# Kernel optimization log

Hardware: AMD Instinct MI355X
Metric: run time of the kernel (lower is better)

The kernel has to match this reference:

```python
import jax, jax.numpy as jnp
import numpy as np

N, D, C = 4096, 512, 64
MARGIN = 1.0
INF = jnp.float32(1e30)


def setup_inputs() -> dict:
    key = jax.random.key(0)
    k1, k2 = jax.random.split(key)
    embeddings = jax.random.normal(k1, (N, D), dtype=jnp.float32)
    targets = jax.random.randint(k2, (N,), 0, C)
    return {"embeddings": embeddings, "targets": targets}


def _triplet_loss(embeddings, targets, margin=MARGIN):
    # Squared pairwise distances [N, N] (differentiable, used for the loss)
    sq_norms = jnp.sum(embeddings * embeddings, axis=1)
    sq_dist = jnp.maximum(
        sq_norms[:, None] + sq_norms[None, :] - 2.0 * (embeddings @ embeddings.T), 0.0
    )
    # Euclidean distances for mining only (index selection is non-differentiable in torch)
    dist = jnp.sqrt(jax.lax.stop_gradient(sq_dist))

    same = targets[:, None] == targets[None, :]  # [N, N] same-label mask

    # Hardest negative per anchor: argmax_k (d_ap - d_ak + margin) == argmin_k d_ak over negatives
    neg_dist = jnp.where(same, INF, dist)
    n_idx = jnp.argmin(neg_dist, axis=1)   # [N] hardest negative index per anchor
    min_neg = jnp.min(neg_dist, axis=1)    # [N] its euclidean distance

    idx = jnp.arange(dist.shape[0])
    # anchor-positive pairs: same label, a < p (torch.combinations on sorted indices)
    pair_mask = same & (idx[:, None] < idx[None, :])
    # triplet kept only if mined loss (euclidean) strictly positive
    valid = pair_mask & (dist - min_neg[:, None] + margin > 0)

    ap_sq = sq_dist                         # [N, N] squared anchor-positive distances
    an_sq = sq_dist[idx, n_idx]             # [N]   squared anchor-hard-negative distances
    losses = jax.nn.relu(ap_sq - an_sq[:, None] + margin)

    cnt = jnp.sum(valid)
    denom = jnp.maximum(cnt, 1).astype(losses.dtype)
    loss = jnp.sum(jnp.where(valid, losses, 0.0)) / denom

    correct = jnp.sum(valid & (ap_sq < an_sq[:, None]))
    accuracy = correct.astype(jnp.float32) / jnp.maximum(cnt, 1).astype(jnp.float32)
    return loss, accuracy


def reference(embeddings, targets):
    return _triplet_loss(embeddings, targets)
```

## Files before the change

### kernel.cpp

```cpp
#include <hip/hip_runtime.h>

#define N 4096
#define D 512
#define C 64
#define MARGIN 1.0f
#define TILE 128
#define ROWB 128
#define NTILES (N / TILE)
#define NTRI (NTILES * (NTILES + 1) / 2)
#define FINF 3.0e38f
#define SLOTW 16
#define PCAP 1024
#define LOSSB 128

typedef __attribute__((ext_vector_type(8))) short short8;
typedef __attribute__((ext_vector_type(4))) float floatx4;

__device__ __forceinline__ unsigned short f2bf(float f) {
  unsigned int u = __float_as_uint(f);
  u += 0x7FFFu + ((u >> 16) & 1u);
  return (unsigned short)(u >> 16);
}

__device__ __forceinline__ void gload_lds16(const void* g, void* l) {
  __builtin_amdgcn_global_load_lds(
      (const __attribute__((address_space(1))) unsigned int*)g,
      (__attribute__((address_space(3))) unsigned int*)l, 16, 0, 0);
}

__global__ __launch_bounds__(256) void prep_kernel(const float* __restrict__ E,
                                                   unsigned short* __restrict__ Ebf,
                                                   float* __restrict__ norms,
                                                   unsigned int* __restrict__ an_sq_bits,
                                                   unsigned int* __restrict__ accs_u,
                                                   unsigned int* __restrict__ ctrl) {
  const int row = blockIdx.x;
  const int tid = threadIdx.x;
  if (row == N) {
    for (int k = tid; k < C * SLOTW; k += 256) accs_u[k] = 0u;
    if (tid < 2) ctrl[tid] = 0u;
    return;
  }
  if (row < 16) an_sq_bits[row * 256 + tid] = 0x7F800000u;
  const float2 v = reinterpret_cast<const float2*>(E + (size_t)row * D)[tid];
  float s = v.x * v.x + v.y * v.y;
  unsigned int packed = ((unsigned int)f2bf(v.y) << 16) | (unsigned int)f2bf(v.x);
  reinterpret_cast<unsigned int*>(Ebf + (size_t)row * D)[tid] = packed;
  for (int off = 32; off > 0; off >>= 1) s += __shfl_down(s, off);
  __shared__ float wsum[4];
  if ((tid & 63) == 0) wsum[tid >> 6] = s;
  __syncthreads();
  if (tid == 0) norms[row] = wsum[0] + wsum[1] + wsum[2] + wsum[3];
}

__global__ __launch_bounds__(256, 3) void gemm_min_kernel(const unsigned short* __restrict__ Ebf,
                                                          const float* __restrict__ norms,
                                                          const int* __restrict__ targets,
                                                          unsigned int* __restrict__ an_sq_bits,
                                                          uint2* __restrict__ pairs,
                                                          unsigned int* __restrict__ ctrl) {
  const int u = blockIdx.x;
  int i = (int)((sqrtf(8.0f * (float)u + 1.0f) - 1.0f) * 0.5f);
  while ((i + 1) * (i + 2) / 2 <= u) ++i;
  while (i * (i + 1) / 2 > u) --i;
  const int tm = u - i * (i + 1) / 2;
  const int tn = i;

  __shared__ alignas(16) unsigned char As[TILE * ROWB];
  __shared__ alignas(16) unsigned char Bs[TILE * ROWB];
  __shared__ float s_rmin[2][TILE];
  __shared__ float s_cmin[2][TILE];
  __shared__ unsigned int s_pkey[PCAP];
  __shared__ float s_psq[PCAP];
  __shared__ unsigned int s_pcnt, s_pbase;

  const int tid = threadIdx.x;
  const int wave = tid >> 6, lane = tid & 63;
  const int quad = lane >> 4, l16 = lane & 15;
  const int wr = wave >> 1, wc = wave & 1;
  const int rowBase = tm * TILE, colBase = tn * TILE;
  if (tid == 0) s_pcnt = 0u;

  const int lr = lane >> 3;
  const int lq = (lane & 7) ^ lr;
  const int lofs = lr * (D * 2) + lq * 16;
  const unsigned char* gA = (const unsigned char*)Ebf + (size_t)rowBase * (D * 2);
  const unsigned char* gB = (const unsigned char*)Ebf + (size_t)colBase * (D * 2);

  const int swz = l16 & 7;
  int rA[4], rB[4], cq[2];
#pragma unroll
  for (int s = 0; s < 4; s++) {
    rA[s] = (wr * 64 + s * 16 + l16) * ROWB;
    rB[s] = (wc * 64 + s * 16 + l16) * ROWB;
  }
#pragma unroll
  for (int ks = 0; ks < 2; ks++) cq[ks] = ((ks * 4 + quad) ^ swz) * 16;

  floatx4 acc[4][4];
#pragma unroll
  for (int a = 0; a < 4; a++)
#pragma unroll
    for (int b = 0; b < 4; b++) acc[a][b] = (floatx4){0.f, 0.f, 0.f, 0.f};

  for (int k0b = 0; k0b < D * 2; k0b += 128) {
#pragma unroll
    for (int t = 0; t < 4; t++) {
      const int g = wave * 4 + t;
      gload_lds16(gA + (size_t)g * 8 * (D * 2) + lofs + k0b, As + g * 1024);
      gload_lds16(gB + (size_t)g * 8 * (D * 2) + lofs + k0b, Bs + g * 1024);
    }
    __syncthreads();
#pragma unroll
    for (int ks = 0; ks < 2; ks++) {
      short8 af[4], bf[4];
#pragma unroll
      for (int s = 0; s < 4; s++) {
        af[s] = *reinterpret_cast<const short8*>(As + rA[s] + cq[ks]);
        bf[s] = *reinterpret_cast<const short8*>(Bs + rB[s] + cq[ks]);
      }
#pragma unroll
      for (int sm = 0; sm < 4; sm++)
#pragma unroll
        for (int sn = 0; sn < 4; sn++)
          acc[sm][sn] = __builtin_amdgcn_mfma_f32_16x16x32_bf16(af[sm], bf[sn], acc[sm][sn], 0, 0, 0);
    }
    __syncthreads();
  }

  int tcol[4], gcolv[4];
  float ncol[4];
#pragma unroll
  for (int sn = 0; sn < 4; sn++) {
    const int gc = colBase + wc * 64 + sn * 16 + l16;
    gcolv[sn] = gc;
    tcol[sn] = targets[gc];
    ncol[sn] = norms[gc];
  }
  float colmin[4] = {FINF, FINF, FINF, FINF};
#pragma unroll
  for (int sm = 0; sm < 4; sm++) {
#pragma unroll
    for (int r = 0; r < 4; r++) {
      const int rloc = wr * 64 + sm * 16 + quad * 4 + r;
      const int grow = rowBase + rloc;
      const int trow = targets[grow];
      const float nrow = norms[grow];
      float rowmin = FINF;
#pragma unroll
      for (int sn = 0; sn < 4; sn++) {
        const float sq = fmaxf(nrow + ncol[sn] - 2.0f * acc[sm][sn][r], 0.0f);
        if (tcol[sn] != trow) {
          rowmin = fminf(rowmin, sq);
          colmin[sn] = fminf(colmin[sn], sq);
        } else if (grow < gcolv[sn]) {
          const unsigned int idx = atomicAdd(&s_pcnt, 1u);
          if (idx < PCAP) {
            s_pkey[idx] = ((unsigned int)grow << 12) | (unsigned int)gcolv[sn];
            s_psq[idx] = sq;
          } else {
            const unsigned int g = atomicAdd(&ctrl[0], 1u);
            pairs[g] = make_uint2(((unsigned int)grow << 12) | (unsigned int)gcolv[sn],
                                  __float_as_uint(sq));
          }
        }
      }
#pragma unroll
      for (int off = 1; off < 16; off <<= 1) rowmin = fminf(rowmin, __shfl_xor(rowmin, off));
      if (l16 == 0) s_rmin[wc][rloc] = rowmin;
    }
  }
#pragma unroll
  for (int sn = 0; sn < 4; sn++) {
    float cm = colmin[sn];
    cm = fminf(cm, __shfl_xor(cm, 16));
    cm = fminf(cm, __shfl_xor(cm, 32));
    if (quad == 0) s_cmin[wr][wc * 64 + sn * 16 + l16] = cm;
  }
  __syncthreads();
  if (tid < TILE) {
    const float m = fminf(s_rmin[0][tid], s_rmin[1][tid]);
    if (m < FINF) atomicMin(&an_sq_bits[rowBase + tid], __float_as_uint(m));
  } else {
    const int c = tid - TILE;
    const float m = fminf(s_cmin[0][c], s_cmin[1][c]);
    if (m < FINF) atomicMin(&an_sq_bits[colBase + c], __float_as_uint(m));
  }
  const unsigned int npair = min(s_pcnt, (unsigned int)PCAP);
  if (tid == 0) s_pbase = atomicAdd(&ctrl[0], npair);
  __syncthreads();
  for (unsigned int r = tid; r < npair; r += 256)
    pairs[s_pbase + r] = make_uint2(s_pkey[r], __float_as_uint(s_psq[r]));
}

__global__ __launch_bounds__(256) void loss_kernel(const uint2* __restrict__ pairs,
                                                   const unsigned int* __restrict__ an_sq_bits,
                                                   float* __restrict__ accs,
                                                   unsigned int* __restrict__ ctrl,
                                                   float* __restrict__ out) {
  const int tid = threadIdx.x, wave = tid >> 6, lane = tid & 63;
  const unsigned int M = ctrl[0];
  __shared__ float s_sum[4];
  __shared__ unsigned int s_cnt[4], s_cor[4];
  __shared__ int s_last;
  float bsum = 0.f;
  unsigned int bcnt = 0, bcor = 0;
  for (unsigned int r = blockIdx.x * 256 + tid; r < M; r += LOSSB * 256) {
    const uint2 rec = pairs[r];
    const int a = (int)(rec.x >> 12);
    const float sq = __uint_as_float(rec.y);
    const float an = __uint_as_float(an_sq_bits[a]);
    if (sqrtf(sq) - sqrtf(an) + MARGIN > 0.0f) {
      bcnt++;
      bsum += fmaxf(sq - an + MARGIN, 0.0f);
      if (sq < an) bcor++;
    }
  }
#pragma unroll
  for (int off = 32; off > 0; off >>= 1) {
    bsum += __shfl_down(bsum, off);
    bcnt += __shfl_down(bcnt, off);
    bcor += __shfl_down(bcor, off);
  }
  if (lane == 0) { s_sum[wave] = bsum; s_cnt[wave] = bcnt; s_cor[wave] = bcor; }
  __syncthreads();
  if (tid == 0) {
    float* slot = accs + (size_t)(blockIdx.x & (C - 1)) * SLOTW;
    atomicAdd(&slot[0], s_sum[0] + s_sum[1] + s_sum[2] + s_sum[3]);
    atomicAdd((unsigned int*)&slot[1], s_cnt[0] + s_cnt[1] + s_cnt[2] + s_cnt[3]);
    atomicAdd((unsigned int*)&slot[2], s_cor[0] + s_cor[1] + s_cor[2] + s_cor[3]);
    __threadfence();
    s_last = (atomicAdd(&ctrl[1], 1u) == (unsigned int)LOSSB - 1u);
  }
  __syncthreads();
  if (s_last) {
    __threadfence();
    if (tid < C) {
      float sum = __uint_as_float(atomicAdd((unsigned int*)&accs[(size_t)tid * SLOTW + 0], 0u));
      unsigned int cnt = atomicAdd((unsigned int*)&accs[(size_t)tid * SLOTW + 1], 0u);
      unsigned int cor = atomicAdd((unsigned int*)&accs[(size_t)tid * SLOTW + 2], 0u);
#pragma unroll
      for (int off = 32; off > 0; off >>= 1) {
        sum += __shfl_down(sum, off);
        cnt += __shfl_down(cnt, off);
        cor += __shfl_down(cor, off);
      }
      if (tid == 0) {
        const float denom = (float)(cnt > 0u ? cnt : 1u);
        out[0] = sum / denom;
        out[1] = (float)cor / denom;
      }
    }
  }
}

extern "C" void kernel_launch(void* const* d_in, const int* in_sizes, int n_in,
                              void* d_out, int out_size, void* d_ws, size_t ws_size,
                              hipStream_t stream) {
  const float* E = (const float*)d_in[0];
  const int* targets = (const int*)d_in[1];
  float* out = (float*)d_out;
  char* ws = (char*)d_ws;
  size_t off = 0;
  unsigned short* Ebf = (unsigned short*)(ws + off); off += (size_t)N * D * 2;
  float* norms = (float*)(ws + off); off += (size_t)N * 4;
  unsigned int* an_sq = (unsigned int*)(ws + off); off += (size_t)N * 4;
  float* accs = (float*)(ws + off); off += (size_t)C * SLOTW * 4;
  unsigned int* ctrl = (unsigned int*)(ws + off); off += 256;
  uint2* pairs = (uint2*)(ws + off);

  prep_kernel<<<dim3(N + 1), dim3(256), 0, stream>>>(E, Ebf, norms, an_sq, (unsigned int*)accs, ctrl);
  gemm_min_kernel<<<dim3(NTRI), dim3(256), 0, stream>>>(Ebf, norms, targets, an_sq, pairs, ctrl);
  loss_kernel<<<dim3(LOSSB), dim3(256), 0, stream>>>(pairs, an_sq, accs, ctrl, out);
}
```

Before: 95.93 us.

## Fuse bf16 conversion and norm computation into the distance GEMM kernel

Result: slower. 137.8 us (+43.6%).

```diff
diff --git a/kernel.cpp b/kernel.cpp
--- a/kernel.cpp
+++ b/kernel.cpp
@@ -5,13 +5,12 @@
 #define C 64
 #define MARGIN 1.0f
 #define TILE 128
-#define ROWB 128
 #define NTILES (N / TILE)
 #define NTRI (NTILES * (NTILES + 1) / 2)
 #define FINF 3.0e38f
 #define SLOTW 16
 #define PCAP 1024
-#define LOSSB 128
+#define LOSSB 132
 
 typedef __attribute__((ext_vector_type(8))) short short8;
 typedef __attribute__((ext_vector_type(4))) float floatx4;
@@ -21,78 +20,56 @@
   u += 0x7FFFu + ((u >> 16) & 1u);
   return (unsigned short)(u >> 16);
 }
-
-__device__ __forceinline__ void gload_lds16(const void* g, void* l) {
-  __builtin_amdgcn_global_load_lds(
-      (const __attribute__((address_space(1))) unsigned int*)g,
-      (__attribute__((address_space(3))) unsigned int*)l, 16, 0, 0);
-}
-
-__global__ __launch_bounds__(256) void prep_kernel(const float* __restrict__ E,
-                                                   unsigned short* __restrict__ Ebf,
-                                                   float* __restrict__ norms,
-                                                   unsigned int* __restrict__ an_sq_bits,
-                                                   unsigned int* __restrict__ accs_u,
-                                                   unsigned int* __restrict__ ctrl) {
-  const int row = blockIdx.x;
-  const int tid = threadIdx.x;
-  if (row == N) {
-    for (int k = tid; k < C * SLOTW; k += 256) accs_u[k] = 0u;
-    if (tid < 2) ctrl[tid] = 0u;
-    return;
-  }
-  if (row < 16) an_sq_bits[row * 256 + tid] = 0x7F800000u;
-  const float2 v = reinterpret_cast<const float2*>(E + (size_t)row * D)[tid];
-  float s = v.x * v.x + v.y * v.y;
-  unsigned int packed = ((unsigned int)f2bf(v.y) << 16) | (unsigned int)f2bf(v.x);
-  reinterpret_cast<unsigned int*>(Ebf + (size_t)row * D)[tid] = packed;
-  for (int off = 32; off > 0; off >>= 1) s += __shfl_down(s, off);
-  __shared__ float wsum[4];
-  if ((tid & 63) == 0) wsum[tid >> 6] = s;
-  __syncthreads();
-  if (tid == 0) norms[row] = wsum[0] + wsum[1] + wsum[2] + wsum[3];
-}
-
-__global__ __launch_bounds__(256, 3) void gemm_min_kernel(const unsigned short* __restrict__ Ebf,
-                                                          const float* __restrict__ norms,
-                                                          const int* __restrict__ targets,
-                                                          unsigned int* __restrict__ an_sq_bits,
-                                                          uint2* __restrict__ pairs,
-                                                          unsigned int* __restrict__ ctrl) {
+__device__ __forceinline__ unsigned int cvt_pk(float x, float y) {
+  return ((unsigned int)f2bf(y) << 16) | (unsigned int)f2bf(x);
+}
+
+__global__ __launch_bounds__(256, 3) void gemm_fused(const float* __restrict__ E,
+                                                     const int* __restrict__ targets,
+                                                     unsigned int* __restrict__ an_key,
+                                                     uint2* __restrict__ pairs,
+                                                     unsigned int* __restrict__ pcnt,
+                                                     unsigned int* __restrict__ accs_u,
+                                                     unsigned int* __restrict__ ctrl) {
   const int u = blockIdx.x;
-  int i = (int)((sqrtf(8.0f * (float)u + 1.0f) - 1.0f) * 0.5f);
-  while ((i + 1) * (i + 2) / 2 <= u) ++i;
-  while (i * (i + 1) / 2 > u) --i;
-  const int tm = u - i * (i + 1) / 2;
-  const int tn = i;
-
-  __shared__ alignas(16) unsigned char As[TILE * ROWB];
-  __shared__ alignas(16) unsigned char Bs[TILE * ROWB];
+  int t = (int)((sqrtf(8.0f * (float)u + 1.0f) - 1.0f) * 0.5f);
+  while ((t + 1) * (t + 2) / 2 <= u) ++t;
+  while (t * (t + 1) / 2 > u) --t;
+  const int tm = u - t * (t + 1) / 2;
+  const int tn = t;
+  const int rowBase = tm * TILE, colBase = tn * TILE;
+
+  __shared__ alignas(16) unsigned char As[TILE * 128];
+  __shared__ alignas(16) unsigned char Bs[TILE * 128];
+  __shared__ float s_normA[TILE], s_normB[TILE];
   __shared__ float s_rmin[2][TILE];
   __shared__ float s_cmin[2][TILE];
   __shared__ unsigned int s_pkey[PCAP];
   __shared__ float s_psq[PCAP];
-  __shared__ unsigned int s_pcnt, s_pbase;
+  __shared__ unsigned int s_pcnt;
 
   const int tid = threadIdx.x;
   const int wave = tid >> 6, lane = tid & 63;
   const int quad = lane >> 4, l16 = lane & 15;
   const int wr = wave >> 1, wc = wave & 1;
-  const int rowBase = tm * TILE, colBase = tn * TILE;
   if (tid == 0) s_pcnt = 0u;
-
-  const int lr = lane >> 3;
-  const int lq = (lane & 7) ^ lr;
-  const int lofs = lr * (D * 2) + lq * 16;
-  const unsigned char* gA = (const unsigned char*)Ebf + (size_t)rowBase * (D * 2);
-  const unsigned char* gB = (const unsigned char*)Ebf + (size_t)colBase * (D * 2);
+  if (u == 0) {
+    for (int k = tid; k < C * SLOTW; k += 256) accs_u[k] = 0u;
+    if (tid < 64) ctrl[tid] = 0u;
+  }
+
+  const int srow = tid >> 1, shalf = tid & 1;
+  const float* gA = E + (size_t)(rowBase + srow) * D + shalf * 32;
+  const float* gB = E + (size_t)(colBase + srow) * D + shalf * 32;
+  const int sswz = srow & 7;
+  float normA = 0.f, normB = 0.f;
 
   const int swz = l16 & 7;
   int rA[4], rB[4], cq[2];
 #pragma unroll
   for (int s = 0; s < 4; s++) {
-    rA[s] = (wr * 64 + s * 16 + l16) * ROWB;
-    rB[s] = (wc * 64 + s * 16 + l16) * ROWB;
+    rA[s] = (wr * 64 + s * 16 + l16) * 128;
+    rB[s] = (wc * 64 + s * 16 + l16) * 128;
   }
 #pragma unroll
   for (int ks = 0; ks < 2; ks++) cq[ks] = ((ks * 4 + quad) ^ swz) * 16;
@@ -103,12 +80,25 @@
 #pragma unroll
     for (int b = 0; b < 4; b++) acc[a][b] = (floatx4){0.f, 0.f, 0.f, 0.f};
 
-  for (int k0b = 0; k0b < D * 2; k0b += 128) {
-#pragma unroll
-    for (int t = 0; t < 4; t++) {
-      const int g = wave * 4 + t;
-      gload_lds16(gA + (size_t)g * 8 * (D * 2) + lofs + k0b, As + g * 1024);
-      gload_lds16(gB + (size_t)g * 8 * (D * 2) + lofs + k0b, Bs + g * 1024);
+  for (int kc = 0; kc < 8; kc++) {
+#pragma unroll
+    for (int jj = 0; jj < 4; jj++) {
+      const float4 a0 = *reinterpret_cast<const float4*>(gA + kc * 64 + jj * 8);
+      const float4 a1 = *reinterpret_cast<const float4*>(gA + kc * 64 + jj * 8 + 4);
+      normA += a0.x * a0.x + a0.y * a0.y + a0.z * a0.z + a0.w * a0.w +
+               a1.x * a1.x + a1.y * a1.y + a1.z * a1.z + a1.w * a1.w;
+      uint4 wa;
+      wa.x = cvt_pk(a0.x, a0.y); wa.y = cvt_pk(a0.z, a0.w);
+      wa.z = cvt_pk(a1.x, a1.y); wa.w = cvt_pk(a1.z, a1.w);
+      *reinterpret_cast<uint4*>(&As[srow * 128 + (((shalf * 4 + jj) ^ sswz) * 16)]) = wa;
+      const float4 b0 = *reinterpret_cast<const float4*>(gB + kc * 64 + jj * 8);
+      const float4 b1 = *reinterpret_cast<const float4*>(gB + kc * 64 + jj * 8 + 4);
+      normB += b0.x * b0.x + b0.y * b0.y + b0.z * b0.z + b0.w * b0.w +
+               b1.x * b1.x + b1.y * b1.y + b1.z * b1.z + b1.w * b1.w;
+      uint4 wb;
+      wb.x = cvt_pk(b0.x, b0.y); wb.y = cvt_pk(b0.z, b0.w);
+      wb.z = cvt_pk(b1.x, b1.y); wb.w = cvt_pk(b1.z, b1.w);
+      *reinterpret_cast<uint4*>(&Bs[srow * 128 + (((shalf * 4 + jj) ^ sswz) * 16)]) = wb;
     }
     __syncthreads();
 #pragma unroll
@@ -128,14 +118,19 @@
     __syncthreads();
   }
 
+  normA += __shfl_xor(normA, 1);
+  normB += __shfl_xor(normB, 1);
+  if (shalf == 0) { s_normA[srow] = normA; s_normB[srow] = normB; }
+  __syncthreads();
+
   int tcol[4], gcolv[4];
   float ncol[4];
 #pragma unroll
   for (int sn = 0; sn < 4; sn++) {
-    const int gc = colBase + wc * 64 + sn * 16 + l16;
-    gcolv[sn] = gc;
-    tcol[sn] = targets[gc];
-    ncol[sn] = norms[gc];
+    const int cloc = wc * 64 + sn * 16 + l16;
+    gcolv[sn] = colBase + cloc;
+    tcol[sn] = targets[gcolv[sn]];
+    ncol[sn] = s_normB[cloc];
   }
   float colmin[4] = {FINF, FINF, FINF, FINF};
 #pragma unroll
@@ -145,7 +140,7 @@
       const int rloc = wr * 64 + sm * 16 + quad * 4 + r;
       const int grow = rowBase + rloc;
       const int trow = targets[grow];
-      const float nrow = norms[grow];
+      const float nrow = s_normA[rloc];
       float rowmin = FINF;
 #pragma unroll
       for (int sn = 0; sn < 4; sn++) {
@@ -158,10 +153,6 @@
           if (idx < PCAP) {
             s_pkey[idx] = ((unsigned int)grow << 12) | (unsigned int)gcolv[sn];
             s_psq[idx] = sq;
-          } else {
-            const unsigned int g = atomicAdd(&ctrl[0], 1u);
-            pairs[g] = make_uint2(((unsigned int)grow << 12) | (unsigned int)gcolv[sn],
-                                  __float_as_uint(sq));
           }
         }
       }
@@ -180,40 +171,43 @@
   __syncthreads();
   if (tid < TILE) {
     const float m = fminf(s_rmin[0][tid], s_rmin[1][tid]);
-    if (m < FINF) atomicMin(&an_sq_bits[rowBase + tid], __float_as_uint(m));
+    if (m < FINF) atomicMax(&an_key[rowBase + tid], ~__float_as_uint(m));
   } else {
     const int c = tid - TILE;
     const float m = fminf(s_cmin[0][c], s_cmin[1][c]);
-    if (m < FINF) atomicMin(&an_sq_bits[colBase + c], __float_as_uint(m));
+    if (m < FINF) atomicMax(&an_key[colBase + c], ~__float_as_uint(m));
   }
   const unsigned int npair = min(s_pcnt, (unsigned int)PCAP);
-  if (tid == 0) s_pbase = atomicAdd(&ctrl[0], npair);
-  __syncthreads();
+  if (tid == 0) pcnt[u] = npair;
   for (unsigned int r = tid; r < npair; r += 256)
-    pairs[s_pbase + r] = make_uint2(s_pkey[r], __float_as_uint(s_psq[r]));
+    pairs[(size_t)u * PCAP + r] = make_uint2(s_pkey[r], __float_as_uint(s_psq[r]));
 }
 
 __global__ __launch_bounds__(256) void loss_kernel(const uint2* __restrict__ pairs,
-                                                   const unsigned int* __restrict__ an_sq_bits,
+                                                   const unsigned int* __restrict__ pcnt,
+                                                   const unsigned int* __restrict__ an_key,
                                                    float* __restrict__ accs,
                                                    unsigned int* __restrict__ ctrl,
                                                    float* __restrict__ out) {
   const int tid = threadIdx.x, wave = tid >> 6, lane = tid & 63;
-  const unsigned int M = ctrl[0];
   __shared__ float s_sum[4];
   __shared__ unsigned int s_cnt[4], s_cor[4];
   __shared__ int s_last;
   float bsum = 0.f;
   unsigned int bcnt = 0, bcor = 0;
-  for (unsigned int r = blockIdx.x * 256 + tid; r < M; r += LOSSB * 256) {
-    const uint2 rec = pairs[r];
-    const int a = (int)(rec.x >> 12);
-    const float sq = __uint_as_float(rec.y);
-    const float an = __uint_as_float(an_sq_bits[a]);
-    if (sqrtf(sq) - sqrtf(an) + MARGIN > 0.0f) {
-      bcnt++;
-      bsum += fmaxf(sq - an + MARGIN, 0.0f);
-      if (sq < an) bcor++;
+  for (int u = blockIdx.x; u < NTRI; u += LOSSB) {
+    const unsigned int n = pcnt[u];
+    const uint2* seg = pairs + (size_t)u * PCAP;
+    for (unsigned int r = tid; r < n; r += 256) {
+      const uint2 rec = seg[r];
+      const int a = (int)(rec.x >> 12);
+      const float sq = __uint_as_float(rec.y);
+      const float an = __uint_as_float(~an_key[a]);
+      if (sqrtf(sq) - sqrtf(an) + MARGIN > 0.0f) {
+        bcnt++;
+        bsum += fmaxf(sq - an + MARGIN, 0.0f);
+        if (sq < an) bcor++;
+      }
     }
   }
 #pragma unroll
@@ -262,14 +256,14 @@
   float* out = (float*)d_out;
   char* ws = (char*)d_ws;
   size_t off = 0;
-  unsigned short* Ebf = (unsigned short*)(ws + off); off += (size_t)N * D * 2;
-  float* norms = (float*)(ws + off); off += (size_t)N * 4;
-  unsigned int* an_sq = (unsigned int*)(ws + off); off += (size_t)N * 4;
+  unsigned int* an_key = (unsigned int*)(ws + off); off += (size_t)N * 4;
   float* accs = (float*)(ws + off); off += (size_t)C * SLOTW * 4;
   unsigned int* ctrl = (unsigned int*)(ws + off); off += 256;
+  unsigned int* pcnt = (unsigned int*)(ws + off); off += (size_t)NTRI * 4;
+  off = (off + 255) & ~(size_t)255;
   uint2* pairs = (uint2*)(ws + off);
 
-  prep_kernel<<<dim3(N + 1), dim3(256), 0, stream>>>(E, Ebf, norms, an_sq, (unsigned int*)accs, ctrl);
-  gemm_min_kernel<<<dim3(NTRI), dim3(256), 0, stream>>>(Ebf, norms, targets, an_sq, pairs, ctrl);
-  loss_kernel<<<dim3(LOSSB), dim3(256), 0, stream>>>(pairs, an_sq, accs, ctrl, out);
-}
+  gemm_fused<<<dim3(NTRI), dim3(256), 0, stream>>>(E, targets, an_key, pairs, pcnt,
+                                                   (unsigned int*)accs, ctrl);
+  loss_kernel<<<dim3(LOSSB), dim3(256), 0, stream>>>(pairs, pcnt, an_key, accs, ctrl, out);
+}
```
